# Optimization experiments

Measured on AMD Instinct MI355X. Metric: run time of the kernel, lower is better.

The kernel has to match this reference:

```python
import jax, jax.numpy as jnp
import numpy as np

K = 5
TAU = 2.0
EPS = 1e-8
SLOPE = 0.2  # LeakyReLU negative slope
BASE = jnp.array([-2.0, -1.0, 0.0, 1.0, 2.0], dtype=jnp.float32)


def _leaky(x):
    return jnp.where(x >= 0, x, SLOPE * x)


def _bilinear1d(feat, x):
    """1D bilinear sample, equivalent to F.grid_sample on an [B,C,1,L] image
    with grid_y=0, padding_mode='border', align_corners=True.
    feat: [B,C,L], x: [B,M] normalized coords in [-1,1]. Returns [B,C,M]."""
    L = feat.shape[-1]
    ix = jnp.clip((x + 1.0) * 0.5 * (L - 1), 0.0, float(L - 1))  # border clamp
    x0 = jnp.floor(ix)
    w = (ix - x0)[:, None, :]  # [B,1,M]
    i0 = jnp.clip(x0.astype(jnp.int32), 0, L - 1)
    i1 = jnp.clip(i0 + 1, 0, L - 1)
    f0 = jnp.take_along_axis(feat, i0[:, None, :], axis=2)
    f1 = jnp.take_along_axis(feat, i1[:, None, :], axis=2)
    return f0 * (1.0 - w) + f1 * w


def setup_inputs() -> dict:
    key = jax.random.key(0)
    ks = jax.random.split(key, 10)
    B, C, Lin, N, H = 4, 256, 4096, 8192, 64
    out_dim = 1 + 1 + K + K  # 12
    feat_1d = jax.random.normal(ks[0], (B, C, Lin), dtype=jnp.float32)
    coords_1d = jax.random.uniform(ks[1], (B, N, 1), minval=-1.0, maxval=1.0, dtype=jnp.float32)
    cell_1d = jnp.full((B, N, 1), 2.0 / Lin, dtype=jnp.float32) * (1.0 + 0.1 * jax.random.uniform(ks[2], (B, N, 1)))
    in_dim = C + 2
    # NOTE: original zero-inits the last linear; we use small random weights to
    # exercise the full computation (non-degenerate offsets/gates).
    W1 = jax.random.normal(ks[3], (in_dim, H), dtype=jnp.float32) * (1.0 / np.sqrt(in_dim))
    b1 = jax.random.normal(ks[4], (H,), dtype=jnp.float32) * 0.01
    Wr = jax.random.normal(ks[5], (H, H), dtype=jnp.float32) * (1.0 / np.sqrt(H))
    br = jax.random.normal(ks[6], (H,), dtype=jnp.float32) * 0.01
    W3 = jax.random.normal(ks[7], (H, out_dim), dtype=jnp.float32) * 0.1
    b3 = jax.random.normal(ks[8], (out_dim,), dtype=jnp.float32) * 0.01
    return {"feat_1d": feat_1d, "coords_1d": coords_1d, "cell_1d": cell_1d,
            "W1": W1, "b1": b1, "Wr": Wr, "br": br, "W3": W3, "b3": b3}


def reference(feat_1d, coords_1d, cell_1d, W1, b1, Wr, br, W3, b3):
    B, C, Lin = feat_1d.shape
    N = coords_1d.shape[1]
    x = coords_1d[..., 0]  # [B,N]
    # anchor features at query coords
    f_anchor = _bilinear1d(feat_1d, x).transpose(0, 2, 1)  # [B,N,C]
    rin = jnp.concatenate([f_anchor, coords_1d, cell_1d], axis=-1)  # [B,N,C+2]
    # router MLP: Linear -> LeakyReLU -> ResidualBlock -> Linear
    h = _leaky(rin @ W1 + b1)
    h = _leaky(h + (h @ Wr + br))
    out = h @ W3 + b3  # [B,N,12]
    r_raw = out[..., 0:1]
    sigma_raw = out[..., 1:2]
    res_raw = out[..., 2:2 + K]
    gate_raw = out[..., 2 + K:2 + 2 * K]
    r = jnp.clip(jax.nn.softplus(r_raw) + 0.3, 0.3, 2.0)          # [B,N,1]
    sigma = jnp.clip(jax.nn.softplus(sigma_raw) + 0.5, 0.5, 3.0)  # [B,N,1]
    res = jnp.tanh(res_raw) * 0.5                                  # [B,N,K]
    off = r * BASE + res                                           # [B,N,K] pixel-unit offsets
    scale_x = 2.0 / max(Lin - 1, 1)
    deform_x = x[:, :, None] + off * scale_x                       # [B,N,K] normalized
    f = _bilinear1d(feat_1d, deform_x.reshape(B, N * K))           # [B,C,N*K]
    f = f.reshape(B, C, N, K).transpose(0, 2, 3, 1)                # [B,N,K,C]
    w_geo = jnp.exp(-0.5 * off ** 2 / ((sigma * TAU) ** 2 + EPS))  # [B,N,K]
    w = w_geo * jax.nn.sigmoid(gate_raw)
    w = w / (w.sum(axis=-1, keepdims=True) + EPS)
    out_feat = jnp.einsum('bnkc,bnk->bnc', f, w)                   # [B,N,C]
    return out_feat
```

## Files before the change

### kernel.cpp

```cpp
#include <hip/hip_runtime.h>
#include <math.h>

#define KK 5
#define C_DIM 256
#define LIN 4096
#define B_DIM 4
#define N_PTS 8192
#define PTS 32

typedef short short8 __attribute__((ext_vector_type(8)));
typedef float f32x4  __attribute__((ext_vector_type(4)));

__device__ __forceinline__ float leaky(float v) { return v >= 0.0f ? v : 0.2f * v; }
__device__ __forceinline__ float softplus_f(float v) { return v > 20.0f ? v : log1pf(expf(v)); }
__device__ __forceinline__ float bflo(unsigned u) { return __uint_as_float(u << 16); }
__device__ __forceinline__ float bfhi(unsigned u) { return __uint_as_float(u & 0xFFFF0000u); }
__device__ __forceinline__ ushort f2bf(float f) {
    unsigned u = __float_as_uint(f);
    u += 0x7FFFu + ((u >> 16) & 1u);
    return (ushort)(u >> 16);
}
__device__ __forceinline__ float bf2f(ushort h) { return __uint_as_float((unsigned)h << 16); }

__global__ __launch_bounds__(256) void prep_weights(
    const float* __restrict__ W1, const float* __restrict__ Wr,
    ushort* __restrict__ W1t_hi, ushort* __restrict__ W1t_lo,
    ushort* __restrict__ Wrt_hi, ushort* __restrict__ Wrt_lo)
{
    int i = blockIdx.x * 256 + threadIdx.x;
    if (i < 64 * 264) {
        int j = i / 264, k = i % 264;
        float v = (k < 256) ? W1[(size_t)k * 64 + j] : 0.0f;
        ushort hi = f2bf(v);
        W1t_hi[i] = hi;
        W1t_lo[i] = f2bf(v - bf2f(hi));
    } else {
        int i2 = i - 64 * 264;
        if (i2 < 64 * 72) {
            int j = i2 / 72, k = i2 % 72;
            float v = (k < 64) ? Wr[(size_t)k * 64 + j] : 0.0f;
            ushort hi = f2bf(v);
            Wrt_hi[i2] = hi;
            Wrt_lo[i2] = f2bf(v - bf2f(hi));
        }
    }
}

__global__ __launch_bounds__(256) void transpose_kernel(
    const float* __restrict__ feat, ushort* __restrict__ feat_t)
{
    __shared__ float tile[32][33];
    int b  = blockIdx.z;
    int l0 = blockIdx.x * 32;
    int c0 = blockIdx.y * 32;
    const float* src = feat + (size_t)b * C_DIM * LIN;
    ushort* dst = feat_t + (size_t)b * LIN * C_DIM;
    int tx = threadIdx.x, ty = threadIdx.y;
#pragma unroll
    for (int i = 0; i < 4; i++)
        tile[ty + i * 8][tx] = src[(size_t)(c0 + ty + i * 8) * LIN + (l0 + tx)];
    __syncthreads();
#pragma unroll
    for (int i = 0; i < 4; i++)
        dst[(size_t)(l0 + ty + i * 8) * C_DIM + (c0 + tx)] = f2bf(tile[tx][ty + i * 8]);
}

__global__ __launch_bounds__(256) void mlp_kernel(
    const ushort* __restrict__ feat_t,
    const float* __restrict__ coords,
    const float* __restrict__ cell,
    const float* __restrict__ W1, const float* __restrict__ b1,
    const float* __restrict__ br,
    const float* __restrict__ W3, const float* __restrict__ b3,
    const ushort* __restrict__ W1t_hi, const ushort* __restrict__ W1t_lo,
    const ushort* __restrict__ Wrt_hi, const ushort* __restrict__ Wrt_lo,
    float* __restrict__ params)
{
    __shared__ ushort Ah[PTS][264], Al[PTS][264];
    __shared__ ushort H1h[PTS][72], H1l[PTS][72];
    __shared__ float  H2[PTS][68];
    __shared__ float  outs[PTS][12];
    __shared__ float  xs[PTS], cls[PTS];

    const int t = threadIdx.x;
    const int base = blockIdx.x * PTS;
    const int bb = base >> 13;
    const ushort* fb = feat_t + (size_t)bb * LIN * C_DIM;

    {
        int p = t >> 3, l8 = t & 7;
        int pt = base + p;
        float x = coords[pt];
        float ix = fminf(fmaxf((x + 1.0f) * 0.5f * (float)(LIN - 1), 0.0f), (float)(LIN - 1));
        float x0 = floorf(ix);
        int i0 = min((int)x0, LIN - 1);
        int i1 = min(i0 + 1, LIN - 1);
        float fr = ix - x0, om = 1.0f - fr;
        if (l8 == 0) { xs[p] = x; cls[p] = cell[pt]; }
        const ushort* r0 = fb + (size_t)i0 * C_DIM;
        const ushort* r1 = fb + (size_t)i1 * C_DIM;
#pragma unroll
        for (int q = 0; q < 4; q++) {
            int c = l8 * 8 + q * 64;
            uint4 u0 = *(const uint4*)(r0 + c);
            uint4 u1 = *(const uint4*)(r1 + c);
            float v[8];
            v[0] = bflo(u0.x) * om + bflo(u1.x) * fr;
            v[1] = bfhi(u0.x) * om + bfhi(u1.x) * fr;
            v[2] = bflo(u0.y) * om + bflo(u1.y) * fr;
            v[3] = bfhi(u0.y) * om + bfhi(u1.y) * fr;
            v[4] = bflo(u0.z) * om + bflo(u1.z) * fr;
            v[5] = bfhi(u0.z) * om + bfhi(u1.z) * fr;
            v[6] = bflo(u0.w) * om + bflo(u1.w) * fr;
            v[7] = bfhi(u0.w) * om + bfhi(u1.w) * fr;
            ushort hv[8], lv[8];
#pragma unroll
            for (int e = 0; e < 8; e++) {
                hv[e] = f2bf(v[e]);
                lv[e] = f2bf(v[e] - bf2f(hv[e]));
            }
            *(uint4*)&Ah[p][c] = *(uint4*)hv;
            *(uint4*)&Al[p][c] = *(uint4*)lv;
        }
    }
    __syncthreads();

    const int wave = t >> 6, lane = t & 63;
    const int cr = lane & 15;
    const int kb = lane >> 4;
    const int jcol = wave * 16 + cr;

    f32x4 acc0 = {0.f, 0.f, 0.f, 0.f}, acc1 = acc0;
    {
        const ushort* B1h = W1t_hi + (size_t)jcol * 264;
        const ushort* B1l = W1t_lo + (size_t)jcol * 264;
#pragma unroll
        for (int k0 = 0; k0 < 256; k0 += 32) {
            int ko = k0 + kb * 8;
            short8 a0h = *(const short8*)&Ah[cr][ko];
            short8 a0l = *(const short8*)&Al[cr][ko];
            short8 a1h = *(const short8*)&Ah[16 + cr][ko];
            short8 a1l = *(const short8*)&Al[16 + cr][ko];
            short8 bh = *(const short8*)(B1h + ko);
            short8 bl = *(const short8*)(B1l + ko);
            acc0 = __builtin_amdgcn_mfma_f32_16x16x32_bf16(a0h, bh, acc0, 0, 0, 0);
            acc0 = __builtin_amdgcn_mfma_f32_16x16x32_bf16(a0h, bl, acc0, 0, 0, 0);
            acc0 = __builtin_amdgcn_mfma_f32_16x16x32_bf16(a0l, bh, acc0, 0, 0, 0);
            acc1 = __builtin_amdgcn_mfma_f32_16x16x32_bf16(a1h, bh, acc1, 0, 0, 0);
            acc1 = __builtin_amdgcn_mfma_f32_16x16x32_bf16(a1h, bl, acc1, 0, 0, 0);
            acc1 = __builtin_amdgcn_mfma_f32_16x16x32_bf16(a1l, bh, acc1, 0, 0, 0);
        }
    }
    float h1a[4], h1b[4];
    {
        float wx = W1[(size_t)256 * 64 + jcol];
        float wc = W1[(size_t)257 * 64 + jcol];
        float bb1 = b1[jcol];
#pragma unroll
        for (int r = 0; r < 4; r++) {
            int p0 = kb * 4 + r;
            float v0 = leaky(acc0[r] + xs[p0] * wx + cls[p0] * wc + bb1);
            h1a[r] = v0;
            ushort hi0 = f2bf(v0);
            H1h[p0][jcol] = hi0;
            H1l[p0][jcol] = f2bf(v0 - bf2f(hi0));
            int p1 = 16 + p0;
            float v1 = leaky(acc1[r] + xs[p1] * wx + cls[p1] * wc + bb1);
            h1b[r] = v1;
            ushort hi1 = f2bf(v1);
            H1h[p1][jcol] = hi1;
            H1l[p1][jcol] = f2bf(v1 - bf2f(hi1));
        }
    }
    __syncthreads();

    f32x4 r0 = {0.f, 0.f, 0.f, 0.f}, r1 = r0;
    {
        const ushort* B2h = Wrt_hi + (size_t)jcol * 72;
        const ushort* B2l = Wrt_lo + (size_t)jcol * 72;
#pragma unroll
        for (int k0 = 0; k0 < 64; k0 += 32) {
            int ko = k0 + kb * 8;
            short8 a0h = *(const short8*)&H1h[cr][ko];
            short8 a0l = *(const short8*)&H1l[cr][ko];
            short8 a1h = *(const short8*)&H1h[16 + cr][ko];
            short8 a1l = *(const short8*)&H1l[16 + cr][ko];
            short8 bh = *(const short8*)(B2h + ko);
            short8 bl = *(const short8*)(B2l + ko);
            r0 = __builtin_amdgcn_mfma_f32_16x16x32_bf16(a0h, bh, r0, 0, 0, 0);
            r0 = __builtin_amdgcn_mfma_f32_16x16x32_bf16(a0h, bl, r0, 0, 0, 0);
            r0 = __builtin_amdgcn_mfma_f32_16x16x32_bf16(a0l, bh, r0, 0, 0, 0);
            r1 = __builtin_amdgcn_mfma_f32_16x16x32_bf16(a1h, bh, r1, 0, 0, 0);
            r1 = __builtin_amdgcn_mfma_f32_16x16x32_bf16(a1h, bl, r1, 0, 0, 0);
            r1 = __builtin_amdgcn_mfma_f32_16x16x32_bf16(a1l, bh, r1, 0, 0, 0);
        }
        float brv = br[jcol];
#pragma unroll
        for (int r = 0; r < 4; r++) {
            int p0 = kb * 4 + r;
            H2[p0][jcol]      = leaky(h1a[r] + r0[r] + brv);
            H2[16 + p0][jcol] = leaky(h1b[r] + r1[r] + brv);
        }
    }
    __syncthreads();

    {
        int p = t & 31;
        int o = t >> 5;
        for (int oo = o; oo < 12; oo += 8) {
            float acc = b3[oo];
#pragma unroll 4
            for (int l = 0; l < 64; l++)
                acc = fmaf(H2[p][l], W3[(size_t)l * 12 + oo], acc);
            outs[p][oo] = acc;
        }
    }
    __syncthreads();

    if (t < PTS) {
        int pt = base + t;
        float x = xs[t];
        float r = softplus_f(outs[t][0]) + 0.3f;
        r = fminf(fmaxf(r, 0.3f), 2.0f);
        float sg = softplus_f(outs[t][1]) + 0.5f;
        sg = fminf(fmaxf(sg, 0.5f), 3.0f);
        float denom = (sg * 2.0f) * (sg * 2.0f) + 1e-8f;
        const float BASEv[KK] = {-2.0f, -1.0f, 0.0f, 1.0f, 2.0f};
        float ixk[KK], wk[KK];
        float wsum = 0.0f;
#pragma unroll
        for (int k = 0; k < KK; k++) {
            float res = tanhf(outs[t][2 + k]) * 0.5f;
            float off = r * BASEv[k] + res;
            float dx = x + off * (2.0f / (float)(LIN - 1));
            float ix = (dx + 1.0f) * 0.5f * (float)(LIN - 1);
            ix = fminf(fmaxf(ix, 0.0f), (float)(LIN - 1));
            float gate = outs[t][2 + KK + k];
            float wgeo = expf(-0.5f * off * off / denom);
            float sig = 1.0f / (1.0f + expf(-gate));
            float w = wgeo * sig;
            ixk[k] = ix; wk[k] = w; wsum += w;
        }
        float inv = 1.0f / (wsum + 1e-8f);
        float* pp = params + (size_t)pt * 10;
#pragma unroll
        for (int k = 0; k < KK; k++) {
            pp[k]     = ixk[k];
            pp[5 + k] = wk[k] * inv;
        }
    }
}

__global__ __launch_bounds__(256) void gather_kernel(
    const ushort* __restrict__ feat_t, const float* __restrict__ params,
    float* __restrict__ out)
{
    int t = threadIdx.x;
    int p = t >> 5;
    int lane = t & 31;
    int pt = blockIdx.x * 8 + p;
    int b = pt >> 13;
    const float* pp = params + (size_t)pt * 10;
    const ushort* fb = feat_t + (size_t)b * LIN * C_DIM;
    int c = lane * 8;
    float a0 = 0, a1 = 0, a2 = 0, a3 = 0, a4 = 0, a5 = 0, a6 = 0, a7 = 0;
#pragma unroll
    for (int k = 0; k < KK; k++) {
        float ix = pp[k];
        float w  = pp[5 + k];
        float x0 = floorf(ix);
        int i0 = (int)x0;
        int i1 = min(i0 + 1, LIN - 1);
        float fr = ix - x0;
        uint4 u0 = *(const uint4*)(fb + (size_t)i0 * C_DIM + c);
        uint4 u1 = *(const uint4*)(fb + (size_t)i1 * C_DIM + c);
        float w0 = w * (1.0f - fr), w1 = w * fr;
        a0 = fmaf(w0, bflo(u0.x), fmaf(w1, bflo(u1.x), a0));
        a1 = fmaf(w0, bfhi(u0.x), fmaf(w1, bfhi(u1.x), a1));
        a2 = fmaf(w0, bflo(u0.y), fmaf(w1, bflo(u1.y), a2));
        a3 = fmaf(w0, bfhi(u0.y), fmaf(w1, bfhi(u1.y), a3));
        a4 = fmaf(w0, bflo(u0.z), fmaf(w1, bflo(u1.z), a4));
        a5 = fmaf(w0, bfhi(u0.z), fmaf(w1, bfhi(u1.z), a5));
        a6 = fmaf(w0, bflo(u0.w), fmaf(w1, bflo(u1.w), a6));
        a7 = fmaf(w0, bfhi(u0.w), fmaf(w1, bfhi(u1.w), a7));
    }
    float* op = out + (size_t)pt * C_DIM + c;
    *(float4*)op       = make_float4(a0, a1, a2, a3);
    *(float4*)(op + 4) = make_float4(a4, a5, a6, a7);
}

extern "C" void kernel_launch(void* const* d_in, const int* in_sizes, int n_in,
                              void* d_out, int out_size, void* d_ws, size_t ws_size,
                              hipStream_t stream) {
    const float* feat   = (const float*)d_in[0];
    const float* coords = (const float*)d_in[1];
    const float* cell   = (const float*)d_in[2];
    const float* W1 = (const float*)d_in[3];
    const float* b1 = (const float*)d_in[4];
    const float* Wr = (const float*)d_in[5];
    const float* br = (const float*)d_in[6];
    const float* W3 = (const float*)d_in[7];
    const float* b3 = (const float*)d_in[8];
    float* out = (float*)d_out;

    char* ws = (char*)d_ws;
    ushort* feat_t = (ushort*)ws;
    ws += (size_t)B_DIM * LIN * C_DIM * 2;
    float* params = (float*)ws;
    ws += (size_t)B_DIM * N_PTS * 10 * 4;
    ushort* W1t_hi = (ushort*)ws; ws += 64 * 264 * 2;
    ushort* W1t_lo = (ushort*)ws; ws += 64 * 264 * 2;
    ushort* Wrt_hi = (ushort*)ws; ws += 64 * 72 * 2;
    ushort* Wrt_lo = (ushort*)ws; ws += 64 * 72 * 2;

    prep_weights<<<(64 * 264 + 64 * 72 + 255) / 256, 256, 0, stream>>>(
        W1, Wr, W1t_hi, W1t_lo, Wrt_hi, Wrt_lo);

    dim3 tb(32, 8);
    dim3 tg(LIN / 32, C_DIM / 32, B_DIM);
    transpose_kernel<<<tg, tb, 0, stream>>>(feat, feat_t);

    int nPts = B_DIM * N_PTS;
    mlp_kernel<<<nPts / PTS, 256, 0, stream>>>(feat_t, coords, cell,
                                               W1, b1, br, W3, b3,
                                               W1t_hi, W1t_lo, Wrt_hi, Wrt_lo,
                                               params);

    gather_kernel<<<nPts / 8, 256, 0, stream>>>(feat_t, params, out);
}
```

Baseline: 128.7 us.

## Counting-sort query points by anchor position to localize gather accesses

Adds a counting sort (histogram, single-block scan, atomic scatter) that orders query points by their anchor pixel index, producing a permutation. The gather kernel then processes points in sorted order, so neighbouring warps read nearby rows of the transposed feature map and should get better L2/cache reuse. In exchange it adds three small kernels plus a memset, an extra indirection per point, and scattered output writes.

```diff
diff --git a/kernel.cpp b/kernel.cpp
--- a/kernel.cpp
+++ b/kernel.cpp
@@ -7,6 +7,7 @@
 #define B_DIM 4
 #define N_PTS 8192
 #define PTS 32
+#define NBUCK (B_DIM * LIN)
 
 typedef short short8 __attribute__((ext_vector_type(8)));
 typedef float f32x4  __attribute__((ext_vector_type(4)));
@@ -21,6 +22,11 @@
     return (ushort)(u >> 16);
 }
 __device__ __forceinline__ float bf2f(ushort h) { return __uint_as_float((unsigned)h << 16); }
+__device__ __forceinline__ int anchor_key(const float* coords, int pt) {
+    float x = coords[pt];
+    float ix = fminf(fmaxf((x + 1.0f) * 0.5f * (float)(LIN - 1), 0.0f), (float)(LIN - 1));
+    return (pt >> 13) * LIN + (int)ix;
+}
 
 __global__ __launch_bounds__(256) void prep_weights(
     const float* __restrict__ W1, const float* __restrict__ Wr,
@@ -46,6 +52,44 @@
     }
 }
 
+__global__ __launch_bounds__(256) void sort_count(
+    const float* __restrict__ coords, unsigned* __restrict__ hist)
+{
+    int pt = blockIdx.x * 256 + threadIdx.x;
+    atomicAdd(&hist[anchor_key(coords, pt)], 1u);
+}
+
+__global__ __launch_bounds__(256) void sort_scan(
+    const unsigned* __restrict__ hist, unsigned* __restrict__ offs)
+{
+    __shared__ unsigned base[256];
+    int t = threadIdx.x;
+    unsigned s = 0;
+    for (int i = 0; i < NBUCK / 256; i++) s += hist[t * (NBUCK / 256) + i];
+    base[t] = s;
+    __syncthreads();
+    if (t == 0) {
+        unsigned run = 0;
+        for (int i = 0; i < 256; i++) { unsigned v = base[i]; base[i] = run; run += v; }
+    }
+    __syncthreads();
+    unsigned run = base[t];
+    for (int i = 0; i < NBUCK / 256; i++) {
+        int idx = t * (NBUCK / 256) + i;
+        offs[idx] = run;
+        run += hist[idx];
+    }
+}
+
+__global__ __launch_bounds__(256) void sort_scatter(
+    const float* __restrict__ coords, unsigned* __restrict__ offs,
+    int* __restrict__ perm)
+{
+    int pt = blockIdx.x * 256 + threadIdx.x;
+    unsigned pos = atomicAdd(&offs[anchor_key(coords, pt)], 1u);
+    perm[pos] = pt;
+}
+
 __global__ __launch_bounds__(256) void transpose_kernel(
     const float* __restrict__ feat, ushort* __restrict__ feat_t)
 {
@@ -253,12 +297,12 @@
 
 __global__ __launch_bounds__(256) void gather_kernel(
     const ushort* __restrict__ feat_t, const float* __restrict__ params,
-    float* __restrict__ out)
+    const int* __restrict__ perm, float* __restrict__ out)
 {
     int t = threadIdx.x;
     int p = t >> 5;
     int lane = t & 31;
-    int pt = blockIdx.x * 8 + p;
+    int pt = perm[blockIdx.x * 8 + p];
     int b = pt >> 13;
     const float* pp = params + (size_t)pt * 10;
     const ushort* fb = feat_t + (size_t)b * LIN * C_DIM;
@@ -312,6 +356,17 @@
     ushort* W1t_lo = (ushort*)ws; ws += 64 * 264 * 2;
     ushort* Wrt_hi = (ushort*)ws; ws += 64 * 72 * 2;
     ushort* Wrt_lo = (ushort*)ws; ws += 64 * 72 * 2;
+    ws = (char*)(((uintptr_t)ws + 255) & ~(uintptr_t)255);
+    unsigned* hist = (unsigned*)ws; ws += NBUCK * 4;
+    unsigned* offs = (unsigned*)ws; ws += NBUCK * 4;
+    int* perm      = (int*)ws;      ws += (size_t)B_DIM * N_PTS * 4;
+
+    int nPts = B_DIM * N_PTS;
+
+    hipMemsetAsync(hist, 0, NBUCK * 4, stream);
+    sort_count<<<nPts / 256, 256, 0, stream>>>(coords, hist);
+    sort_scan<<<1, 256, 0, stream>>>(hist, offs);
+    sort_scatter<<<nPts / 256, 256, 0, stream>>>(coords, offs, perm);
 
     prep_weights<<<(64 * 264 + 64 * 72 + 255) / 256, 256, 0, stream>>>(
         W1, Wr, W1t_hi, W1t_lo, Wrt_hi, Wrt_lo);
@@ -320,11 +375,10 @@
     dim3 tg(LIN / 32, C_DIM / 32, B_DIM);
     transpose_kernel<<<tg, tb, 0, stream>>>(feat, feat_t);
 
-    int nPts = B_DIM * N_PTS;
     mlp_kernel<<<nPts / PTS, 256, 0, stream>>>(feat_t, coords, cell,
                                                W1, b1, br, W3, b3,
                                                W1t_hi, W1t_lo, Wrt_hi, Wrt_lo,
                                                params);
 
-    gather_kernel<<<nPts / 8, 256, 0, stream>>>(feat_t, params, out);
-}
+    gather_kernel<<<nPts / 8, 256, 0, stream>>>(feat_t, params, perm, out);
+}
```

New measurement: 144.1 us. 12.0% more time.
